# Optimization experiments

Hardware: AMD Instinct MI355X
Metric: run time of the kernel (lower is better)

The kernel has to match this reference:

```python
import jax, jax.numpy as jnp
import numpy as np

N = 16384   # num_nodes (also in_channels: identity-style features)
C = 256     # hidden channels
K = 16      # num_classes
E = 524288  # num edges


def gcn_conv(x, src, dst, ew, W, b, num_nodes):
    """PyG GCNConv: linear transform, then sym-normalized scatter-add aggregation.
    Self-loops (weight 1) are appended; norm = d^-1/2[src] * w * d^-1/2[dst]."""
    h = x @ W                                            # [N, out]
    loop = jnp.arange(num_nodes, dtype=src.dtype)
    s = jnp.concatenate([src, loop])
    d = jnp.concatenate([dst, loop])
    w = jnp.concatenate([ew, jnp.ones((num_nodes,), ew.dtype)])
    deg = jax.ops.segment_sum(w, d, num_segments=num_nodes)
    dinv = jnp.where(deg > 0, jax.lax.rsqrt(jnp.maximum(deg, 1e-12)), 0.0)
    norm = dinv[s] * w * dinv[d]                         # [E+N]
    msg = norm[:, None] * h[s]                           # gather + scale
    out = jax.ops.segment_sum(msg, d, num_segments=num_nodes)  # scatter-add
    return out + b


def setup_inputs() -> dict:
    key = jax.random.key(0)
    k1, k2, k3, k4, k5, k6, k7 = jax.random.split(key, 7)
    x = jax.random.normal(k1, (N, N), dtype=jnp.float32)
    edge_index = jax.random.randint(k2, (2, E), 0, N, dtype=jnp.int64)
    edge_weight = jax.random.uniform(k3, (E,), dtype=jnp.float32)
    # GCNConv parameters (glorot-ish scale)
    W1 = jax.random.normal(k4, (N, C), dtype=jnp.float32) / np.sqrt(N)
    b1 = jnp.zeros((C,), jnp.float32)
    W2 = jax.random.normal(k5, (C, K), dtype=jnp.float32) / np.sqrt(C)
    b2 = jnp.zeros((K,), jnp.float32)
    return {"x": x, "edge_index": edge_index, "edge_weight": edge_weight,
            "W1": W1, "b1": b1, "W2": W2, "b2": b2}


def reference(x, edge_index, edge_weight, W1, b1, W2, b2):
    src, dst = edge_index[0], edge_index[1]
    h = gcn_conv(x, src, dst, edge_weight, W1, b1, N)
    h = jax.nn.relu(h)
    # dropout p=0.5 is identity in eval mode (self.training == False)
    out = gcn_conv(h, src, dst, edge_weight, W2, b2, N)
    return out
```

## Files before the change

kernel.cpp:

```cpp
#include <hip/hip_runtime.h>
#include <stdint.h>


namespace {
constexpr int NN = 16384;
constexpr int CH = 256;
constexpr int KC = 16;
constexpr int NE = 524288;
constexpr int KD = 16384;
constexpr int KSPLIT = 4;
constexpr int BM = 128;

constexpr size_t OFF_W1T  = 0;
constexpr size_t OFF_HP   = 8388608;
constexpr size_t OFF_HB   = 75497472;
constexpr size_t OFF_OUT1 = 83886080;
constexpr size_t OFF_H2   = 100663296;
constexpr size_t OFF_DEG  = 101711872;
constexpr size_t OFF_CNT  = 101777408;
constexpr size_t OFF_DINV = 101842944;
constexpr size_t OFF_ROWP = 101908480;
constexpr size_t OFF_CUR  = 102039552;
constexpr size_t OFF_COLS = 102105088;
constexpr size_t OFF_NRM  = 104202240;
}

typedef __attribute__((ext_vector_type(8))) short bf16x8;
typedef __attribute__((ext_vector_type(4))) float f32x4;

__device__ __forceinline__ unsigned short f2bf(float f) {
  unsigned int u = __builtin_bit_cast(unsigned int, f);
  u += 0x7fffu + ((u >> 16) & 1u);
  return (unsigned short)(u >> 16);
}
__device__ __forceinline__ float bf2f(unsigned short v) {
  unsigned int u = ((unsigned int)v) << 16;
  return __builtin_bit_cast(float, u);
}

__global__ __launch_bounds__(256)
void k_w1t(const float* __restrict__ w1, unsigned short* __restrict__ w1t) {
  __shared__ float tile[64][65];
  const int t = threadIdx.x;
  const int kb = blockIdx.x * 64;
  const int nb = blockIdx.y * 64;
  const int r = t >> 6;
  const int c = t & 63;
#pragma unroll
  for (int i = 0; i < 16; ++i)
    tile[i * 4 + r][c] = w1[(size_t)(kb + i * 4 + r) * CH + nb + c];
  __syncthreads();
#pragma unroll
  for (int i = 0; i < 16; ++i)
    w1t[(size_t)(nb + i * 4 + r) * KD + kb + c] = f2bf(tile[c][i * 4 + r]);
}

__global__ __launch_bounds__(256)
void k_deg(const int* __restrict__ dst, const float* __restrict__ ew,
           float* __restrict__ deg, int* __restrict__ cnt) {
  const int e = blockIdx.x * 256 + threadIdx.x;
  const int d = dst[e];
  atomicAdd(&deg[d], ew[e]);
  atomicAdd(&cnt[d], 1);
}

__global__ __launch_bounds__(256)
void k_dinv(const float* __restrict__ deg, float* __restrict__ dinv) {
  const int i = blockIdx.x * 256 + threadIdx.x;
  dinv[i] = rsqrtf(deg[i] + 1.0f);
}

__global__ __launch_bounds__(256)
void k_scan(const int* __restrict__ cnt, int* __restrict__ rowp, int* __restrict__ curs) {
  __shared__ int ps[256];
  const int t = threadIdx.x;
  const int base = t * 64;
  int s = 0;
  for (int j = 0; j < 64; ++j) s += cnt[base + j];
  ps[t] = s;
  __syncthreads();
  int v = s;
  for (int off = 1; off < 256; off <<= 1) {
    int u = (t >= off) ? ps[t - off] : 0;
    __syncthreads();
    v += u;
    ps[t] = v;
    __syncthreads();
  }
  int run = v - s;
  for (int j = 0; j < 64; ++j) {
    int c = cnt[base + j];
    rowp[base + j] = run;
    curs[base + j] = run;
    run += c;
  }
  if (t == 255) rowp[NN] = run;
}

__global__ __launch_bounds__(256)
void k_fill(const int* __restrict__ src, const int* __restrict__ dst,
            const float* __restrict__ ew, const float* __restrict__ dinv,
            int* __restrict__ curs, int* __restrict__ cols, float* __restrict__ nrm) {
  const int e = blockIdx.x * 256 + threadIdx.x;
  const int s = src[e], d = dst[e];
  const int pos = atomicAdd(&curs[d], 1);
  cols[pos] = s;
  nrm[pos] = dinv[s] * ew[e] * dinv[d];
}

__global__ __launch_bounds__(256, 2)
void k_gemm1(const float* __restrict__ x, const unsigned short* __restrict__ w1t,
             float* __restrict__ hp) {
  __shared__ __align__(16) unsigned short As[2][BM * 32];
  __shared__ __align__(16) unsigned short Bs[2][256 * 32];

  const int tid  = threadIdx.x;
  const int lane = tid & 63;
  const int wave = tid >> 6;

  const int bid  = blockIdx.x;
  const int xcd  = bid & 7;
  const int slot = bid >> 3;
  const int kb   = xcd >> 1;
  const int bm0  = (slot * 2 + (xcd & 1)) * BM;
  const int koff = kb * (KD / KSPLIT);
  const int wn0  = wave * 64;

  const int r0  = tid >> 2;
  const int kq  = tid & 3;
  const int acn = kq ^ ((r0 >> 1) & 3);
  const int aoff0 = r0 * 32 + acn * 8;
  const int aoff1 = (r0 + 64) * 32 + acn * 8;

  const int cc = (lane & 3) ^ ((lane >> 3) & 3);
  const unsigned short* bbase =
      w1t + (size_t)(wave * 64 + (lane >> 2)) * KD + koff + cc * 8;

  const int fr = lane & 15, fg = lane >> 4;
  const int fch = fg ^ ((fr >> 1) & 3);
  const int fA = fr * 32 + fch * 8;
  const int fB = (wn0 + fr) * 32 + fch * 8;

  const float* xrow0 = x + (size_t)(bm0 + r0) * KD + koff + kq * 8;
  const float* xrow1 = xrow0 + (size_t)64 * KD;

  float4 a00, a01, a10, a11;
  f32x4 acc[8][4] = {};

  auto GLOADB = [&](int t, int buf) {
    const unsigned short* g = bbase + (size_t)t * 32;
#pragma unroll
    for (int i = 0; i < 4; ++i) {
      __builtin_amdgcn_global_load_lds(
          (const __attribute__((address_space(1))) void*)(g + (size_t)i * 16 * KD),
          (__attribute__((address_space(3))) void*)(&Bs[buf][(wave * 64 + i * 16) * 32]),
          16, 0, 0);
    }
  };
  auto LOADA = [&](int t) {
    const float* p0 = xrow0 + (size_t)t * 32;
    const float* p1 = xrow1 + (size_t)t * 32;
    a00 = *reinterpret_cast<const float4*>(p0);
    a01 = *reinterpret_cast<const float4*>(p0 + 4);
    a10 = *reinterpret_cast<const float4*>(p1);
    a11 = *reinterpret_cast<const float4*>(p1 + 4);
  };
  auto STOREA = [&](int buf) {
    bf16x8 v;
    v[0] = (short)f2bf(a00.x); v[1] = (short)f2bf(a00.y);
    v[2] = (short)f2bf(a00.z); v[3] = (short)f2bf(a00.w);
    v[4] = (short)f2bf(a01.x); v[5] = (short)f2bf(a01.y);
    v[6] = (short)f2bf(a01.z); v[7] = (short)f2bf(a01.w);
    *reinterpret_cast<bf16x8*>(&As[buf][aoff0]) = v;
    v[0] = (short)f2bf(a10.x); v[1] = (short)f2bf(a10.y);
    v[2] = (short)f2bf(a10.z); v[3] = (short)f2bf(a10.w);
    v[4] = (short)f2bf(a11.x); v[5] = (short)f2bf(a11.y);
    v[6] = (short)f2bf(a11.z); v[7] = (short)f2bf(a11.w);
    *reinterpret_cast<bf16x8*>(&As[buf][aoff1]) = v;
  };

  constexpr int NT = KD / KSPLIT / 32;
  GLOADB(0, 0);
  LOADA(0);
  STOREA(0);
  __syncthreads();
  int cur = 0;

  for (int t = 0; t < NT; ++t) {
    if (t + 1 < NT) {
      GLOADB(t + 1, cur ^ 1);
      LOADA(t + 1);
    }
    bf16x8 bfr[4];
#pragma unroll
    for (int ni = 0; ni < 4; ++ni)
      bfr[ni] = *reinterpret_cast<const bf16x8*>(&Bs[cur][fB + ni * 512]);
    __builtin_amdgcn_s_setprio(1);
#pragma unroll
    for (int mi = 0; mi < 8; ++mi) {
      const bf16x8 af = *reinterpret_cast<const bf16x8*>(&As[cur][fA + mi * 512]);
#pragma unroll
      for (int ni = 0; ni < 4; ++ni)
        acc[mi][ni] = __builtin_amdgcn_mfma_f32_16x16x32_bf16(af, bfr[ni], acc[mi][ni], 0, 0, 0);
    }
    __builtin_amdgcn_s_setprio(0);
    if (t + 1 < NT) {
      STOREA(cur ^ 1);
      __syncthreads();
      cur ^= 1;
    }
  }

  float* hpo = hp + (size_t)kb * NN * CH;
#pragma unroll
  for (int mi = 0; mi < 8; ++mi)
#pragma unroll
    for (int ni = 0; ni < 4; ++ni)
#pragma unroll
      for (int r = 0; r < 4; ++r) {
        const int m = bm0 + mi * 16 + fg * 4 + r;
        const int n = wn0 + ni * 16 + fr;
        hpo[(size_t)m * CH + n] = acc[mi][ni][r];
      }
}

__global__ __launch_bounds__(256)
void k_hred(const float* __restrict__ hp, unsigned short* __restrict__ hb) {
  const size_t i = ((size_t)blockIdx.x * 256 + threadIdx.x) * 8;
  float s[8];
#pragma unroll
  for (int j = 0; j < 8; ++j) s[j] = 0.f;
#pragma unroll
  for (int p = 0; p < KSPLIT; ++p) {
    const float* q = hp + (size_t)p * NN * CH + i;
    const float4 v0 = *reinterpret_cast<const float4*>(q);
    const float4 v1 = *reinterpret_cast<const float4*>(q + 4);
    s[0] += v0.x; s[1] += v0.y; s[2] += v0.z; s[3] += v0.w;
    s[4] += v1.x; s[5] += v1.y; s[6] += v1.z; s[7] += v1.w;
  }
  bf16x8 o;
#pragma unroll
  for (int j = 0; j < 8; ++j) o[j] = (short)f2bf(s[j]);
  *reinterpret_cast<bf16x8*>(hb + i) = o;
}

__global__ __launch_bounds__(256)
void k_agg1(const unsigned short* __restrict__ hb, const int* __restrict__ rowp,
            const int* __restrict__ cols, const float* __restrict__ nrm,
            const float* __restrict__ dinv, const float* __restrict__ b1,
            float* __restrict__ out1) {
  __shared__ float red[4][256];
  const int i = blockIdx.x;
  const int t = threadIdx.x;
  const int w = t >> 6, l = t & 63;
  const int beg = rowp[i], end = rowp[i + 1];
  float a0 = 0.f, a1 = 0.f, a2 = 0.f, a3 = 0.f;
  int e = beg + w;
  for (; e + 4 < end; e += 8) {
    const int s0 = cols[e], s1 = cols[e + 4];
    const float n0 = nrm[e], n1 = nrm[e + 4];
    const ushort4 h0 = *reinterpret_cast<const ushort4*>(hb + (size_t)s0 * CH + l * 4);
    const ushort4 h1 = *reinterpret_cast<const ushort4*>(hb + (size_t)s1 * CH + l * 4);
    a0 += n0 * bf2f(h0.x) + n1 * bf2f(h1.x);
    a1 += n0 * bf2f(h0.y) + n1 * bf2f(h1.y);
    a2 += n0 * bf2f(h0.z) + n1 * bf2f(h1.z);
    a3 += n0 * bf2f(h0.w) + n1 * bf2f(h1.w);
  }
  if (e < end) {
    const int s0 = cols[e];
    const float n0 = nrm[e];
    const ushort4 h0 = *reinterpret_cast<const ushort4*>(hb + (size_t)s0 * CH + l * 4);
    a0 += n0 * bf2f(h0.x); a1 += n0 * bf2f(h0.y);
    a2 += n0 * bf2f(h0.z); a3 += n0 * bf2f(h0.w);
  }
  *reinterpret_cast<float4*>(&red[w][l * 4]) = make_float4(a0, a1, a2, a3);
  __syncthreads();
  const float di = dinv[i];
  float sum = red[0][t] + red[1][t] + red[2][t] + red[3][t]
            + di * di * bf2f(hb[(size_t)i * CH + t]) + b1[t];
  out1[(size_t)i * CH + t] = fmaxf(sum, 0.0f);
}

__global__ __launch_bounds__(256)
void k_gemm2(const float* __restrict__ out1, const float* __restrict__ w2,
             float* __restrict__ h2) {
  __shared__ float xs[16][256];
  __shared__ float ws[256 * 16];
  const int t = threadIdx.x;
  const int n0 = blockIdx.x * 16;
#pragma unroll
  for (int i = 0; i < 16; ++i) ws[i * 256 + t] = w2[i * 256 + t];
#pragma unroll
  for (int i = 0; i < 16; ++i) xs[i][t] = out1[(size_t)(n0 + i) * CH + t];
  __syncthreads();
  const int node = t >> 4, k = t & 15;
  float acc = 0.f;
#pragma unroll 8
  for (int c = 0; c < 256; ++c) acc += xs[node][c] * ws[c * 16 + k];
  h2[(size_t)(n0 + node) * KC + k] = acc;
}

__global__ __launch_bounds__(256)
void k_agg2(const float* __restrict__ h2, const int* __restrict__ rowp,
            const int* __restrict__ cols, const float* __restrict__ nrm,
            const float* __restrict__ dinv, const float* __restrict__ b2,
            float* __restrict__ out) {
  const int i = blockIdx.x * 4 + (threadIdx.x >> 6);
  const int lane = threadIdx.x & 63;
  const int k = lane & 15, g = lane >> 4;
  const int beg = rowp[i], end = rowp[i + 1];
  float acc = 0.f;
  for (int e = beg + g; e < end; e += 4)
    acc += nrm[e] * h2[(size_t)cols[e] * KC + k];
  acc += __shfl_xor(acc, 16);
  acc += __shfl_xor(acc, 32);
  if (g == 0) {
    const float di = dinv[i];
    out[(size_t)i * KC + k] = acc + di * di * h2[(size_t)i * KC + k] + b2[k];
  }
}

extern "C" void kernel_launch(void* const* d_in, const int* in_sizes, int n_in,
                              void* d_out, int out_size, void* d_ws, size_t ws_size,
                              hipStream_t stream) {
  const float* x  = (const float*)d_in[0];
  const int*   ei = (const int*)d_in[1];
  const float* ew = (const float*)d_in[2];
  const float* w1 = (const float*)d_in[3];
  const float* b1 = (const float*)d_in[4];
  const float* w2 = (const float*)d_in[5];
  const float* b2 = (const float*)d_in[6];
  const int* src = ei;
  const int* dst = ei + NE;

  uint8_t* ws = (uint8_t*)d_ws;
  unsigned short* w1t = (unsigned short*)(ws + OFF_W1T);
  float* hp   = (float*)(ws + OFF_HP);
  unsigned short* hb = (unsigned short*)(ws + OFF_HB);
  float* out1 = (float*)(ws + OFF_OUT1);
  float* h2   = (float*)(ws + OFF_H2);
  float* deg  = (float*)(ws + OFF_DEG);
  int*   cnt  = (int*)(ws + OFF_CNT);
  float* dinv = (float*)(ws + OFF_DINV);
  int*   rowp = (int*)(ws + OFF_ROWP);
  int*   curs = (int*)(ws + OFF_CUR);
  int*   cols = (int*)(ws + OFF_COLS);
  float* nrm  = (float*)(ws + OFF_NRM);
  float* out  = (float*)d_out;

  hipMemsetAsync(ws + OFF_DEG, 0, 131072, stream);

  k_w1t <<<dim3(256, 4), 256, 0, stream>>>(w1, w1t);
  k_deg <<<NE / 256, 256, 0, stream>>>(dst, ew, deg, cnt);
  k_dinv<<<NN / 256, 256, 0, stream>>>(deg, dinv);
  k_scan<<<1, 256, 0, stream>>>(cnt, rowp, curs);
  k_fill<<<NE / 256, 256, 0, stream>>>(src, dst, ew, dinv, curs, cols, nrm);
  k_gemm1<<<(NN / BM) * KSPLIT, 256, 0, stream>>>(x, w1t, hp);
  k_hred<<<NN * CH / (256 * 8), 256, 0, stream>>>(hp, hb);
  k_agg1<<<NN, 256, 0, stream>>>(hb, rowp, cols, nrm, dinv, b1, out1);
  k_gemm2<<<NN / 16, 256, 0, stream>>>(out1, w2, h2);
  k_agg2<<<NN / 4, 256, 0, stream>>>(h2, rowp, cols, nrm, dinv, b2, out);
}
```

Before: 469.0 us.

## Deepen gemm1 to a 4-stage direct-to-LDS pipeline and fold dinv into scan

The main GEMM now streams both the fp32 activation tile and the bf16 weight tile straight into LDS with global_load_lds. It keeps three tiles in flight across a 4-buffer ring, synchronised with explicit vmcnt waits and barriers. The fp32-to-bf16 conversion moves from a register staging step to the point where fragments are read from LDS. Blocks grow to 512 threads arranged as a 2x4 wave grid. Separately, the dinv computation is merged into the single-block scan kernel to drop one launch. The trade-offs: 128KB of LDS per block limits occupancy, the tail iterations issue redundant wrapped loads, and twice the A bytes now pass through LDS.

New measurement: 499.9 us. 6.6% more time.

```diff
diff --git a/kernel.cpp b/kernel.cpp
--- a/kernel.cpp
+++ b/kernel.cpp
@@ -10,6 +10,9 @@
 constexpr int KD = 16384;
 constexpr int KSPLIT = 4;
 constexpr int BM = 128;
+constexpr int NT = KD / KSPLIT / 32;
+constexpr int ABYTES = BM * 128;
+constexpr int BBYTES = 256 * 64;
 
 constexpr size_t OFF_W1T  = 0;
 constexpr size_t OFF_HP   = 8388608;
@@ -65,19 +68,17 @@
 }
 
 __global__ __launch_bounds__(256)
-void k_dinv(const float* __restrict__ deg, float* __restrict__ dinv) {
-  const int i = blockIdx.x * 256 + threadIdx.x;
-  dinv[i] = rsqrtf(deg[i] + 1.0f);
-}
-
-__global__ __launch_bounds__(256)
-void k_scan(const int* __restrict__ cnt, int* __restrict__ rowp, int* __restrict__ curs) {
+void k_scan(const int* __restrict__ cnt, const float* __restrict__ deg,
+            int* __restrict__ rowp, int* __restrict__ curs,
+            float* __restrict__ dinv) {
   __shared__ int ps[256];
   const int t = threadIdx.x;
   const int base = t * 64;
   int s = 0;
   for (int j = 0; j < 64; ++j) s += cnt[base + j];
   ps[t] = s;
+  for (int j = 0; j < 64; ++j)
+    dinv[base + j] = rsqrtf(deg[base + j] + 1.0f);
   __syncthreads();
   int v = s;
   for (int off = 1; off < 256; off <<= 1) {
@@ -108,15 +109,16 @@
   nrm[pos] = dinv[s] * ew[e] * dinv[d];
 }
 
-__global__ __launch_bounds__(256, 2)
+__global__ __launch_bounds__(512, 2)
 void k_gemm1(const float* __restrict__ x, const unsigned short* __restrict__ w1t,
              float* __restrict__ hp) {
-  __shared__ __align__(16) unsigned short As[2][BM * 32];
-  __shared__ __align__(16) unsigned short Bs[2][256 * 32];
+  __shared__ __align__(16) uint8_t lds[4][ABYTES + BBYTES];
 
   const int tid  = threadIdx.x;
   const int lane = tid & 63;
   const int wave = tid >> 6;
+  const int wm   = wave >> 2;
+  const int wn   = wave & 3;
 
   const int bid  = blockIdx.x;
   const int xcd  = bid & 7;
@@ -124,102 +126,83 @@
   const int kb   = xcd >> 1;
   const int bm0  = (slot * 2 + (xcd & 1)) * BM;
   const int koff = kb * (KD / KSPLIT);
-  const int wn0  = wave * 64;
-
-  const int r0  = tid >> 2;
-  const int kq  = tid & 3;
-  const int acn = kq ^ ((r0 >> 1) & 3);
-  const int aoff0 = r0 * 32 + acn * 8;
-  const int aoff1 = (r0 + 64) * 32 + acn * 8;
-
-  const int cc = (lane & 3) ^ ((lane >> 3) & 3);
-  const unsigned short* bbase =
-      w1t + (size_t)(wave * 64 + (lane >> 2)) * KD + koff + cc * 8;
+
+  const float* asrc0 = x + (size_t)(bm0 + 8 * wave + (lane >> 3)) * KD + koff
+                         + (((lane & 7) ^ (lane >> 3)) << 2);
+  const float* asrc1 = asrc0 + (size_t)64 * KD;
+  const unsigned short* bsrc0 = w1t + (size_t)(16 * wave + (lane >> 2)) * KD + koff
+                                    + (((lane & 3) ^ ((lane >> 3) & 3)) << 3);
+  const unsigned short* bsrc1 = bsrc0 + (size_t)128 * KD;
 
   const int fr = lane & 15, fg = lane >> 4;
-  const int fch = fg ^ ((fr >> 1) & 3);
-  const int fA = fr * 32 + fch * 8;
-  const int fB = (wn0 + fr) * 32 + fch * 8;
-
-  const float* xrow0 = x + (size_t)(bm0 + r0) * KD + koff + kq * 8;
-  const float* xrow1 = xrow0 + (size_t)64 * KD;
-
-  float4 a00, a01, a10, a11;
-  f32x4 acc[8][4] = {};
-
-  auto GLOADB = [&](int t, int buf) {
-    const unsigned short* g = bbase + (size_t)t * 32;
-#pragma unroll
-    for (int i = 0; i < 4; ++i) {
-      __builtin_amdgcn_global_load_lds(
-          (const __attribute__((address_space(1))) void*)(g + (size_t)i * 16 * KD),
-          (__attribute__((address_space(3))) void*)(&Bs[buf][(wave * 64 + i * 16) * 32]),
-          16, 0, 0);
-    }
+  const int aoff = (((2 * fg) ^ (fr & 7)) << 4);
+  const int boff = ((fg ^ ((fr >> 1) & 3)) << 4);
+  const int arow = (wm * 64 + fr) * 128 + aoff;
+  const int brow = ABYTES + (wn * 64 + fr) * 64 + boff;
+
+  f32x4 acc[4][4] = {};
+
+  auto ISSUE = [&](int tile, int buf) {
+    uint8_t* base = &lds[buf][0];
+    const float* ap0 = asrc0 + (size_t)tile * 32;
+    const float* ap1 = asrc1 + (size_t)tile * 32;
+    const unsigned short* bp0 = bsrc0 + (size_t)tile * 32;
+    const unsigned short* bp1 = bsrc1 + (size_t)tile * 32;
+    __builtin_amdgcn_global_load_lds(
+        (const __attribute__((address_space(1))) void*)ap0,
+        (__attribute__((address_space(3))) void*)(base + wave * 1024), 16, 0, 0);
+    __builtin_amdgcn_global_load_lds(
+        (const __attribute__((address_space(1))) void*)ap1,
+        (__attribute__((address_space(3))) void*)(base + (wave + 8) * 1024), 16, 0, 0);
+    __builtin_amdgcn_global_load_lds(
+        (const __attribute__((address_space(1))) void*)bp0,
+        (__attribute__((address_space(3))) void*)(base + ABYTES + wave * 1024), 16, 0, 0);
+    __builtin_amdgcn_global_load_lds(
+        (const __attribute__((address_space(1))) void*)bp1,
+        (__attribute__((address_space(3))) void*)(base + ABYTES + 8192 + wave * 1024), 16, 0, 0);
   };
-  auto LOADA = [&](int t) {
-    const float* p0 = xrow0 + (size_t)t * 32;
-    const float* p1 = xrow1 + (size_t)t * 32;
-    a00 = *reinterpret_cast<const float4*>(p0);
-    a01 = *reinterpret_cast<const float4*>(p0 + 4);
-    a10 = *reinterpret_cast<const float4*>(p1);
-    a11 = *reinterpret_cast<const float4*>(p1 + 4);
-  };
-  auto STOREA = [&](int buf) {
-    bf16x8 v;
-    v[0] = (short)f2bf(a00.x); v[1] = (short)f2bf(a00.y);
-    v[2] = (short)f2bf(a00.z); v[3] = (short)f2bf(a00.w);
-    v[4] = (short)f2bf(a01.x); v[5] = (short)f2bf(a01.y);
-    v[6] = (short)f2bf(a01.z); v[7] = (short)f2bf(a01.w);
-    *reinterpret_cast<bf16x8*>(&As[buf][aoff0]) = v;
-    v[0] = (short)f2bf(a10.x); v[1] = (short)f2bf(a10.y);
-    v[2] = (short)f2bf(a10.z); v[3] = (short)f2bf(a10.w);
-    v[4] = (short)f2bf(a11.x); v[5] = (short)f2bf(a11.y);
-    v[6] = (short)f2bf(a11.z); v[7] = (short)f2bf(a11.w);
-    *reinterpret_cast<bf16x8*>(&As[buf][aoff1]) = v;
-  };
-
-  constexpr int NT = KD / KSPLIT / 32;
-  GLOADB(0, 0);
-  LOADA(0);
-  STOREA(0);
-  __syncthreads();
-  int cur = 0;
+
+  ISSUE(0, 0);
+  ISSUE(1, 1);
+  ISSUE(2, 2);
 
   for (int t = 0; t < NT; ++t) {
-    if (t + 1 < NT) {
-      GLOADB(t + 1, cur ^ 1);
-      LOADA(t + 1);
-    }
+    int t3 = t + 3; if (t3 >= NT) t3 -= NT;
+    ISSUE(t3, (t + 3) & 3);
+    asm volatile("s_waitcnt vmcnt(12)" ::: "memory");
+    asm volatile("s_barrier" ::: "memory");
+    const uint8_t* Ab = &lds[t & 3][0];
     bf16x8 bfr[4];
 #pragma unroll
     for (int ni = 0; ni < 4; ++ni)
-      bfr[ni] = *reinterpret_cast<const bf16x8*>(&Bs[cur][fB + ni * 512]);
+      bfr[ni] = *reinterpret_cast<const bf16x8*>(Ab + brow + ni * 1024);
     __builtin_amdgcn_s_setprio(1);
 #pragma unroll
-    for (int mi = 0; mi < 8; ++mi) {
-      const bf16x8 af = *reinterpret_cast<const bf16x8*>(&As[cur][fA + mi * 512]);
+    for (int mi = 0; mi < 4; ++mi) {
+      const f32x4 lo = *reinterpret_cast<const f32x4*>(Ab + arow + mi * 2048);
+      const f32x4 hi = *reinterpret_cast<const f32x4*>(Ab + ((arow + mi * 2048) ^ 16));
+      bf16x8 af;
+      af[0] = (short)f2bf(lo[0]); af[1] = (short)f2bf(lo[1]);
+      af[2] = (short)f2bf(lo[2]); af[3] = (short)f2bf(lo[3]);
+      af[4] = (short)f2bf(hi[0]); af[5] = (short)f2bf(hi[1]);
+      af[6] = (short)f2bf(hi[2]); af[7] = (short)f2bf(hi[3]);
 #pragma unroll
       for (int ni = 0; ni < 4; ++ni)
         acc[mi][ni] = __builtin_amdgcn_mfma_f32_16x16x32_bf16(af, bfr[ni], acc[mi][ni], 0, 0, 0);
     }
     __builtin_amdgcn_s_setprio(0);
-    if (t + 1 < NT) {
-      STOREA(cur ^ 1);
-      __syncthreads();
-      cur ^= 1;
-    }
+    asm volatile("s_barrier" ::: "memory");
   }
 
   float* hpo = hp + (size_t)kb * NN * CH;
 #pragma unroll
-  for (int mi = 0; mi < 8; ++mi)
+  for (int mi = 0; mi < 4; ++mi)
 #pragma unroll
     for (int ni = 0; ni < 4; ++ni)
 #pragma unroll
       for (int r = 0; r < 4; ++r) {
-        const int m = bm0 + mi * 16 + fg * 4 + r;
-        const int n = wn0 + ni * 16 + fr;
+        const int m = bm0 + wm * 64 + mi * 16 + fg * 4 + r;
+        const int n = wn * 64 + ni * 16 + fr;
         hpo[(size_t)m * CH + n] = acc[mi][ni][r];
       }
 }
@@ -352,10 +335,9 @@
 
   k_w1t <<<dim3(256, 4), 256, 0, stream>>>(w1, w1t);
   k_deg <<<NE / 256, 256, 0, stream>>>(dst, ew, deg, cnt);
-  k_dinv<<<NN / 256, 256, 0, stream>>>(deg, dinv);
-  k_scan<<<1, 256, 0, stream>>>(cnt, rowp, curs);
+  k_scan<<<1, 256, 0, stream>>>(cnt, deg, rowp, curs, dinv);
   k_fill<<<NE / 256, 256, 0, stream>>>(src, dst, ew, dinv, curs, cols, nrm);
-  k_gemm1<<<(NN / BM) * KSPLIT, 256, 0, stream>>>(x, w1t, hp);
+  k_gemm1<<<(NN / BM) * KSPLIT, 512, 0, stream>>>(x, w1t, hp);
   k_hred<<<NN * CH / (256 * 8), 256, 0, stream>>>(hp, hb);
   k_agg1<<<NN, 256, 0, stream>>>(hb, rowp, cols, nrm, dinv, b1, out1);
   k_gemm2<<<NN / 16, 256, 0, stream>>>(out1, w2, h2);
```

## Deepen GEMM1 A-prefetch to two stages and fold dinv into scan kernel

Applied to the files above, without the earlier changes.

The GEMM1 main loop is restructured into a manually unrolled pair of iterations with two register sets for the fp32 A tile. Global loads of A are issued two K-steps ahead, and the LDS store of the previous prefetch happens before compute, so more global latency is hidden behind the MFMAs. The separate dinv kernel is merged into the single-block scan kernel, which removes one launch. The cost is more live registers, which may reduce occupancy, and the dinv computation becomes serial work inside a single block.

New measurement: 1.049 ms. 124% more time.

```diff
diff --git a/kernel.cpp b/kernel.cpp
--- a/kernel.cpp
+++ b/kernel.cpp
@@ -10,6 +10,7 @@
 constexpr int KD = 16384;
 constexpr int KSPLIT = 4;
 constexpr int BM = 128;
+constexpr int NT = KD / KSPLIT / 32;
 
 constexpr size_t OFF_W1T  = 0;
 constexpr size_t OFF_HP   = 8388608;
@@ -65,19 +66,17 @@
 }
 
 __global__ __launch_bounds__(256)
-void k_dinv(const float* __restrict__ deg, float* __restrict__ dinv) {
-  const int i = blockIdx.x * 256 + threadIdx.x;
-  dinv[i] = rsqrtf(deg[i] + 1.0f);
-}
-
-__global__ __launch_bounds__(256)
-void k_scan(const int* __restrict__ cnt, int* __restrict__ rowp, int* __restrict__ curs) {
+void k_scan(const int* __restrict__ cnt, const float* __restrict__ deg,
+            int* __restrict__ rowp, int* __restrict__ curs,
+            float* __restrict__ dinv) {
   __shared__ int ps[256];
   const int t = threadIdx.x;
   const int base = t * 64;
   int s = 0;
   for (int j = 0; j < 64; ++j) s += cnt[base + j];
   ps[t] = s;
+  for (int j = 0; j < 64; ++j)
+    dinv[base + j] = rsqrtf(deg[base + j] + 1.0f);
   __syncthreads();
   int v = s;
   for (int off = 1; off < 256; off <<= 1) {
@@ -144,9 +143,33 @@
   const float* xrow0 = x + (size_t)(bm0 + r0) * KD + koff + kq * 8;
   const float* xrow1 = xrow0 + (size_t)64 * KD;
 
-  float4 a00, a01, a10, a11;
   f32x4 acc[8][4] = {};
 
+  float4 sa0, sa1, sa2, sa3;
+  float4 sb0, sb1, sb2, sb3;
+
+  auto LOADA = [&](int t, float4& v0, float4& v1, float4& v2, float4& v3) {
+    const float* p0 = xrow0 + (size_t)t * 32;
+    const float* p1 = xrow1 + (size_t)t * 32;
+    v0 = *reinterpret_cast<const float4*>(p0);
+    v1 = *reinterpret_cast<const float4*>(p0 + 4);
+    v2 = *reinterpret_cast<const float4*>(p1);
+    v3 = *reinterpret_cast<const float4*>(p1 + 4);
+  };
+  auto STOREA = [&](int buf, const float4& v0, const float4& v1,
+                    const float4& v2, const float4& v3) {
+    bf16x8 v;
+    v[0] = (short)f2bf(v0.x); v[1] = (short)f2bf(v0.y);
+    v[2] = (short)f2bf(v0.z); v[3] = (short)f2bf(v0.w);
+    v[4] = (short)f2bf(v1.x); v[5] = (short)f2bf(v1.y);
+    v[6] = (short)f2bf(v1.z); v[7] = (short)f2bf(v1.w);
+    *reinterpret_cast<bf16x8*>(&As[buf][aoff0]) = v;
+    v[0] = (short)f2bf(v2.x); v[1] = (short)f2bf(v2.y);
+    v[2] = (short)f2bf(v2.z); v[3] = (short)f2bf(v2.w);
+    v[4] = (short)f2bf(v3.x); v[5] = (short)f2bf(v3.y);
+    v[6] = (short)f2bf(v3.z); v[7] = (short)f2bf(v3.w);
+    *reinterpret_cast<bf16x8*>(&As[buf][aoff1]) = v;
+  };
   auto GLOADB = [&](int t, int buf) {
     const unsigned short* g = bbase + (size_t)t * 32;
 #pragma unroll
@@ -157,40 +180,8 @@
           16, 0, 0);
     }
   };
-  auto LOADA = [&](int t) {
-    const float* p0 = xrow0 + (size_t)t * 32;
-    const float* p1 = xrow1 + (size_t)t * 32;
-    a00 = *reinterpret_cast<const float4*>(p0);
-    a01 = *reinterpret_cast<const float4*>(p0 + 4);
-    a10 = *reinterpret_cast<const float4*>(p1);
-    a11 = *reinterpret_cast<const float4*>(p1 + 4);
-  };
-  auto STOREA = [&](int buf) {
-    bf16x8 v;
-    v[0] = (short)f2bf(a00.x); v[1] = (short)f2bf(a00.y);
-    v[2] = (short)f2bf(a00.z); v[3] = (short)f2bf(a00.w);
-    v[4] = (short)f2bf(a01.x); v[5] = (short)f2bf(a01.y);
-    v[6] = (short)f2bf(a01.z); v[7] = (short)f2bf(a01.w);
-    *reinterpret_cast<bf16x8*>(&As[buf][aoff0]) = v;
-    v[0] = (short)f2bf(a10.x); v[1] = (short)f2bf(a10.y);
-    v[2] = (short)f2bf(a10.z); v[3] = (short)f2bf(a10.w);
-    v[4] = (short)f2bf(a11.x); v[5] = (short)f2bf(a11.y);
-    v[6] = (short)f2bf(a11.z); v[7] = (short)f2bf(a11.w);
-    *reinterpret_cast<bf16x8*>(&As[buf][aoff1]) = v;
-  };
-
-  constexpr int NT = KD / KSPLIT / 32;
-  GLOADB(0, 0);
-  LOADA(0);
-  STOREA(0);
-  __syncthreads();
-  int cur = 0;
-
-  for (int t = 0; t < NT; ++t) {
-    if (t + 1 < NT) {
-      GLOADB(t + 1, cur ^ 1);
-      LOADA(t + 1);
-    }
+  auto COMPUTE = [&](int t) {
+    const int cur = t & 1;
     bf16x8 bfr[4];
 #pragma unroll
     for (int ni = 0; ni < 4; ++ni)
@@ -204,10 +195,33 @@
         acc[mi][ni] = __builtin_amdgcn_mfma_f32_16x16x32_bf16(af, bfr[ni], acc[mi][ni], 0, 0, 0);
     }
     __builtin_amdgcn_s_setprio(0);
-    if (t + 1 < NT) {
-      STOREA(cur ^ 1);
+  };
+
+  LOADA(0, sa0, sa1, sa2, sa3);
+  STOREA(0, sa0, sa1, sa2, sa3);
+  GLOADB(0, 0);
+  LOADA(1, sb0, sb1, sb2, sb3);
+  __syncthreads();
+
+  for (int t = 0; t < NT; t += 2) {
+    {
+      STOREA((t + 1) & 1, sb0, sb1, sb2, sb3);
+      if (t + 2 < NT) LOADA(t + 2, sa0, sa1, sa2, sa3);
+      GLOADB(t + 1, (t + 1) & 1);
+      COMPUTE(t);
       __syncthreads();
-      cur ^= 1;
+    }
+    {
+      const int u = t + 1;
+      if (u + 1 < NT) {
+        STOREA((u + 1) & 1, sa0, sa1, sa2, sa3);
+        if (u + 2 < NT) LOADA(u + 2, sb0, sb1, sb2, sb3);
+        GLOADB(u + 1, (u + 1) & 1);
+        COMPUTE(u);
+        __syncthreads();
+      } else {
+        COMPUTE(u);
+      }
     }
   }
 
@@ -352,8 +366,7 @@
 
   k_w1t <<<dim3(256, 4), 256, 0, stream>>>(w1, w1t);
   k_deg <<<NE / 256, 256, 0, stream>>>(dst, ew, deg, cnt);
-  k_dinv<<<NN / 256, 256, 0, stream>>>(deg, dinv);
-  k_scan<<<1, 256, 0, stream>>>(cnt, rowp, curs);
+  k_scan<<<1, 256, 0, stream>>>(cnt, deg, rowp, curs, dinv);
   k_fill<<<NE / 256, 256, 0, stream>>>(src, dst, ew, dinv, curs, cols, nrm);
   k_gemm1<<<(NN / BM) * KSPLIT, 256, 0, stream>>>(x, w1t, hp);
   k_hred<<<NN * CH / (256 * 8), 256, 0, stream>>>(hp, hb);
```
